# Performance work log

Hardware: AMD Instinct MI355X
Metric: run time of the kernel (lower is better)

Reference implementation:

```python
import jax, jax.numpy as jnp
import numpy as np

N = 100000      # nodes
E = 1600000     # edges
H = 128         # hidden_dim
L = 4           # num_layers (blocks AND inner GGC steps)
G = 512         # graphs in batch
IN = 128        # input_dim
OUT = 16        # output_dim
HS = H // 2     # mlp hidden


def setup_inputs() -> dict:
    key = jax.random.key(0)
    ks = jax.random.split(key, 24)
    s = 0.05
    inp = {
        "node_embed": jax.random.normal(ks[0], (N, IN), dtype=jnp.float32),
        "edge_index": jax.random.randint(ks[1], (2, E), 0, N, dtype=jnp.int32),
        "batch": jnp.sort(jax.random.randint(ks[2], (N,), 0, G, dtype=jnp.int32)),
        # nodeEmbed Linear
        "node_w": jax.random.normal(ks[3], (H, IN), dtype=jnp.float32) * s,
        "node_b": jnp.zeros((H,), dtype=jnp.float32),
        # per-block GatedGraphConv weights: [blocks, steps, H, H]
        "ggc_weight": jax.random.normal(ks[4], (L, L, H, H), dtype=jnp.float32) * s,
        # per-block GRUCell weights (torch layout: [3H, H], gates r,z,n)
        "gru_w_ih": jax.random.normal(ks[5], (L, 3 * H, H), dtype=jnp.float32) * s,
        "gru_w_hh": jax.random.normal(ks[6], (L, 3 * H, H), dtype=jnp.float32) * s,
        "gru_b_ih": jnp.zeros((L, 3 * H), dtype=jnp.float32),
        "gru_b_hh": jnp.zeros((L, 3 * H), dtype=jnp.float32),
        # cat_linear: H*L -> H
        "cat_w": jax.random.normal(ks[7], (H, H * L), dtype=jnp.float32) * s,
        "cat_b": jnp.zeros((H,), dtype=jnp.float32),
        # gate_nn: H -> 1
        "gate_w": jax.random.normal(ks[8], (1, H), dtype=jnp.float32) * s,
        "gate_b": jnp.zeros((1,), dtype=jnp.float32),
        # mlp
        "mlp_w1": jax.random.normal(ks[9], (HS, H), dtype=jnp.float32) * s,
        "mlp_b1": jnp.zeros((HS,), dtype=jnp.float32),
        "mlp_w2": jax.random.normal(ks[10], (HS, HS), dtype=jnp.float32) * s,
        "mlp_b2": jnp.zeros((HS,), dtype=jnp.float32),
        # heads
        "out_w": jax.random.normal(ks[11], (OUT, HS), dtype=jnp.float32) * s,
        "out_b": jnp.zeros((OUT,), dtype=jnp.float32),
        "line_w": jax.random.normal(ks[12], (OUT, H), dtype=jnp.float32) * s,
        "line_b": jnp.zeros((OUT,), dtype=jnp.float32),
    }
    return inp


def _gru_cell(m, h, w_ih, w_hh, b_ih, b_hh):
    gi = m @ w_ih.T + b_ih            # [N, 3H]
    gh = h @ w_hh.T + b_hh            # [N, 3H]
    i_r, i_z, i_n = jnp.split(gi, 3, axis=-1)
    h_r, h_z, h_n = jnp.split(gh, 3, axis=-1)
    r = jax.nn.sigmoid(i_r + h_r)
    z = jax.nn.sigmoid(i_z + h_z)
    n = jnp.tanh(i_n + r * h_n)
    return (1.0 - z) * n + z * h


def _gated_graph_conv(x, src, dst, W, w_ih, w_hh, b_ih, b_hh):
    n = x.shape[0]
    for i in range(W.shape[0]):       # fixed small step count
        m = x @ W[i]                  # [N, H]
        agg = jax.ops.segment_sum(m[src], dst, num_segments=n)  # scatter-add messages
        x = _gru_cell(agg, x, w_ih, w_hh, b_ih, b_hh)
    return x


def reference(node_embed, edge_index, batch, node_w, node_b, ggc_weight,
              gru_w_ih, gru_w_hh, gru_b_ih, gru_b_hh, cat_w, cat_b,
              gate_w, gate_b, mlp_w1, mlp_b1, mlp_w2, mlp_b2,
              out_w, out_b, line_w, line_b):
    src, dst = edge_index[0], edge_index[1]
    h0 = node_embed @ node_w.T + node_b                     # nodeEmbed
    # all residual blocks consume the SAME h0 (per original forward loop)
    outs = [
        _gated_graph_conv(h0, src, dst, ggc_weight[k], gru_w_ih[k],
                          gru_w_hh[k], gru_b_ih[k], gru_b_hh[k]) + h0
        for k in range(ggc_weight.shape[0])
    ]
    hidden = jnp.concatenate(outs, axis=-1) @ cat_w.T + cat_b  # [N, H]
    lineout = hidden @ line_w.T + line_b                       # [N, OUT]
    # attentional aggregation: scatter softmax over per-graph gates
    gate = (hidden @ gate_w.T + gate_b)[:, 0]                  # [N]
    gmax = jax.ops.segment_max(gate, batch, num_segments=G)
    ex = jnp.exp(gate - gmax[batch])
    denom = jax.ops.segment_sum(ex, batch, num_segments=G)
    alpha = ex / denom[batch]
    pooled = jax.ops.segment_sum(alpha[:, None] * hidden, batch, num_segments=G)  # [G, H]
    h = jax.nn.relu(pooled @ mlp_w1.T + mlp_b1)
    h = jax.nn.relu(h @ mlp_w2.T + mlp_b2)
    out = h @ out_w.T + out_b                                  # [G, OUT]
    return (out, lineout)
```

## Files before the change

kernel.cpp:

```cpp
#include <hip/hip_runtime.h>

#define N_NODES 100000
#define N_EDGES 1600000
#define HD 128
#define NH (N_NODES * HD)

typedef __attribute__((ext_vector_type(8))) short bf16x8;
typedef __attribute__((ext_vector_type(4))) float f32x4;

__device__ inline unsigned short f2bf(float f) {
  unsigned u = __float_as_uint(f);
  unsigned r = (u + 0x7FFFu + ((u >> 16) & 1u)) >> 16;
  return (unsigned short)r;
}
__device__ inline float bf2f(unsigned short b) {
  return __uint_as_float(((unsigned)b) << 16);
}
__device__ inline float sigm_f(float x) {
  return __builtin_amdgcn_rcpf(1.f + __expf(-x));
}
__device__ inline float tanh_f(float x) {
  return 1.f - 2.f * __builtin_amdgcn_rcpf(__expf(2.f * x) + 1.f);
}

__global__ __launch_bounds__(256) void gemm_h0_k(
    const float* __restrict__ A, const float* __restrict__ B,
    const float* __restrict__ bias, unsigned short* __restrict__ Cb, int M) {
  __shared__ float As[16][132];
  __shared__ float Bs[16][68];
  const int tid = threadIdx.x;
  const int row0 = blockIdx.x * 128;
  const int col0 = blockIdx.y * 64;
  const int tx = tid & 15, ty = tid >> 4;

  float acc[8][4];
#pragma unroll
  for (int i = 0; i < 8; i++)
#pragma unroll
    for (int j = 0; j < 4; j++) acc[i][j] = 0.f;

  const int lr = tid >> 2;
  const int kg = (tid & 3) * 4;

  for (int k0 = 0; k0 < 128; k0 += 16) {
#pragma unroll
    for (int h = 0; h < 2; ++h) {
      int r = lr + h * 64;
      float4 v = make_float4(0.f, 0.f, 0.f, 0.f);
      if (row0 + r < M)
        v = *reinterpret_cast<const float4*>(A + (size_t)(row0 + r) * 128 + k0 + kg);
      As[kg + 0][r] = v.x;
      As[kg + 1][r] = v.y;
      As[kg + 2][r] = v.z;
      As[kg + 3][r] = v.w;
    }
    {
      int c = lr;
      float4 v = *reinterpret_cast<const float4*>(B + (size_t)(col0 + c) * 128 + k0 + kg);
      Bs[kg + 0][c] = v.x;
      Bs[kg + 1][c] = v.y;
      Bs[kg + 2][c] = v.z;
      Bs[kg + 3][c] = v.w;
    }
    __syncthreads();
#pragma unroll
    for (int kk = 0; kk < 16; ++kk) {
      float a[8], b[4];
#pragma unroll
      for (int i = 0; i < 8; i++) a[i] = As[kk][ty * 8 + i];
#pragma unroll
      for (int j = 0; j < 4; j++) b[j] = Bs[kk][tx * 4 + j];
#pragma unroll
      for (int i = 0; i < 8; i++)
#pragma unroll
        for (int j = 0; j < 4; j++) acc[i][j] += a[i] * b[j];
    }
    __syncthreads();
  }

#pragma unroll
  for (int i = 0; i < 8; i++) {
    int r = row0 + ty * 8 + i;
    if (r < M) {
#pragma unroll
      for (int j = 0; j < 4; j++) {
        int c = col0 + tx * 4 + j;
        Cb[(size_t)r * 128 + c] = f2bf(acc[i][j] + bias[c]);
      }
    }
  }
}

__global__ __launch_bounds__(256) void gemm_wct_k(
    const float* __restrict__ w_ih, const float* __restrict__ ggc_w,
    float* __restrict__ Cout) {
  const int z = blockIdx.z;
  const float* A = w_ih + (size_t)(z >> 2) * 384 * 128;
  const float* B = ggc_w + (size_t)z * 128 * 128;
  float* C = Cout + (size_t)z * 384 * 128;
  __shared__ float As[16][132];
  __shared__ float Bs[16][68];
  const int tid = threadIdx.x;
  const int row0 = blockIdx.x * 128;
  const int col0 = blockIdx.y * 64;
  const int tx = tid & 15, ty = tid >> 4;

  float acc[8][4];
#pragma unroll
  for (int i = 0; i < 8; i++)
#pragma unroll
    for (int j = 0; j < 4; j++) acc[i][j] = 0.f;

  const int lr = tid >> 2;
  const int kg = (tid & 3) * 4;

  for (int k0 = 0; k0 < 128; k0 += 16) {
#pragma unroll
    for (int h = 0; h < 2; ++h) {
      int r = lr + h * 64;
      float4 v = *reinterpret_cast<const float4*>(A + (size_t)(row0 + r) * 128 + k0 + kg);
      As[kg + 0][r] = v.x;
      As[kg + 1][r] = v.y;
      As[kg + 2][r] = v.z;
      As[kg + 3][r] = v.w;
    }
    {
      int c = lr;
      float4 v = *reinterpret_cast<const float4*>(B + (size_t)(col0 + c) * 128 + k0 + kg);
      Bs[kg + 0][c] = v.x;
      Bs[kg + 1][c] = v.y;
      Bs[kg + 2][c] = v.z;
      Bs[kg + 3][c] = v.w;
    }
    __syncthreads();
#pragma unroll
    for (int kk = 0; kk < 16; ++kk) {
      float a[8], b[4];
#pragma unroll
      for (int i = 0; i < 8; i++) a[i] = As[kk][ty * 8 + i];
#pragma unroll
      for (int j = 0; j < 4; j++) b[j] = Bs[kk][tx * 4 + j];
#pragma unroll
      for (int i = 0; i < 8; i++)
#pragma unroll
        for (int j = 0; j < 4; j++) acc[i][j] += a[i] * b[j];
    }
    __syncthreads();
  }

#pragma unroll
  for (int i = 0; i < 8; i++) {
    int r = row0 + ty * 8 + i;
#pragma unroll
    for (int j = 0; j < 4; j++) {
      int c = col0 + tx * 4 + j;
      C[(size_t)r * 128 + c] = acc[i][j];
    }
  }
}

__global__ __launch_bounds__(256) void f2b_k(const float* __restrict__ a,
                                             unsigned short* __restrict__ b, int n) {
  int i = blockIdx.x * 256 + threadIdx.x;
  if (i * 4 >= n) return;
  float4 v = reinterpret_cast<const float4*>(a)[i];
  ushort4 o;
  o.x = f2bf(v.x);
  o.y = f2bf(v.y);
  o.z = f2bf(v.z);
  o.w = f2bf(v.w);
  reinterpret_cast<ushort4*>(b)[i] = o;
}

template <bool LAST>
__global__ __launch_bounds__(256) void gru_mfma5_k(
    const unsigned short* __restrict__ agg_base, size_t agg_zs,
    const unsigned short* __restrict__ xb_base, size_t xstride,
    const unsigned short* __restrict__ h0b,
    const unsigned short* __restrict__ wct_base, size_t wct_zs,
    const unsigned short* __restrict__ whh_base, size_t whh_zs,
    const float* __restrict__ bih_base, const float* __restrict__ bhh_base,
    unsigned short* __restrict__ xbout, int nRowTiles) {
  const int z = blockIdx.z;
  const unsigned short* agg = agg_base + (size_t)z * agg_zs;
  const unsigned short* xb = xb_base + (size_t)z * xstride;
  unsigned short* out = xbout + (size_t)z * NH;
  const unsigned short* wctb = wct_base + (size_t)z * wct_zs;
  const unsigned short* whhb = whh_base + (size_t)z * whh_zs;
  const float* b_ih = bih_base + z * 384;
  const float* b_hh = bhh_base + z * 384;

  const int lane = threadIdx.x & 63;
  const int wave = threadIdx.x >> 6;
  const int lrow = lane & 15;
  const int kblk = lane >> 4;
  const int c = blockIdx.y * 16 + lrow;

  bf16x8 wf[6][4];
#pragma unroll
  for (int s = 0; s < 3; s++)
#pragma unroll
    for (int kk = 0; kk < 4; kk++) {
      size_t off = (size_t)(s * 128 + c) * 128 + kk * 32 + kblk * 8;
      wf[s][kk] = *reinterpret_cast<const bf16x8*>(wctb + off);
      wf[s + 3][kk] = *reinterpret_cast<const bf16x8*>(whhb + off);
    }
  const float bi0 = b_ih[c], bi1 = b_ih[128 + c], bi2 = b_ih[256 + c];
  const float bh0 = b_hh[c], bh1 = b_hh[128 + c], bh2 = b_hh[256 + c];

  const int tstride = gridDim.x * 4;
  for (int rt = blockIdx.x * 4 + wave; rt < nRowTiles; rt += tstride) {
    const int row0 = rt * 16;
    const size_t abase = (size_t)(row0 + lrow) * 128 + kblk * 8;
    const int ob = row0 + kblk * 4;

    unsigned short hxv[4], h0v[4];
#pragma unroll
    for (int r = 0; r < 4; r++) {
      hxv[r] = xb[(size_t)(ob + r) * 128 + c];
      if (LAST) h0v[r] = h0b[(size_t)(ob + r) * 128 + c];
    }

    f32x4 acc[6];
#pragma unroll
    for (int s = 0; s < 6; s++) acc[s] = (f32x4)(0.f);
#pragma unroll
    for (int kk = 0; kk < 4; kk++) {
      bf16x8 a_ag = *reinterpret_cast<const bf16x8*>(agg + abase + kk * 32);
      bf16x8 a_x = *reinterpret_cast<const bf16x8*>(xb + abase + kk * 32);
      acc[0] = __builtin_amdgcn_mfma_f32_16x16x32_bf16(a_ag, wf[0][kk], acc[0], 0, 0, 0);
      acc[1] = __builtin_amdgcn_mfma_f32_16x16x32_bf16(a_ag, wf[1][kk], acc[1], 0, 0, 0);
      acc[2] = __builtin_amdgcn_mfma_f32_16x16x32_bf16(a_ag, wf[2][kk], acc[2], 0, 0, 0);
      acc[3] = __builtin_amdgcn_mfma_f32_16x16x32_bf16(a_x, wf[3][kk], acc[3], 0, 0, 0);
      acc[4] = __builtin_amdgcn_mfma_f32_16x16x32_bf16(a_x, wf[4][kk], acc[4], 0, 0, 0);
      acc[5] = __builtin_amdgcn_mfma_f32_16x16x32_bf16(a_x, wf[5][kk], acc[5], 0, 0, 0);
    }
#pragma unroll
    for (int r = 0; r < 4; r++) {
      size_t idx = (size_t)(ob + r) * 128 + c;
      float ir = acc[0][r] + bi0;
      float iz = acc[1][r] + bi1;
      float in_ = acc[2][r] + bi2;
      float hr = acc[3][r] + bh0;
      float hz = acc[4][r] + bh1;
      float hn = acc[5][r] + bh2;
      float rg = sigm_f(ir + hr);
      float zg = sigm_f(iz + hz);
      float ng = tanh_f(in_ + rg * hn);
      float h = bf2f(hxv[r]);
      float nv = (1.f - zg) * ng + zg * h;
      if (LAST) nv += bf2f(h0v[r]);
      out[idx] = f2bf(nv);
    }
  }
}

__global__ __launch_bounds__(256) void cat_mfma2_k(
    const unsigned short* __restrict__ outs, const unsigned short* __restrict__ wcatb,
    const float* __restrict__ cat_b, float* __restrict__ hidden, int M, int pair) {
  const int lane = threadIdx.x & 63;
  const int wave = threadIdx.x >> 6;
  const int row0 = blockIdx.x * 64 + wave * 16;
  const int c0 = blockIdx.y * 32;
  const int lrow = lane & 15;
  const int kb = lane >> 4;
  int arow = row0 + lrow;
  if (arow >= M) arow = M - 1;

  f32x4 acc[2];
  acc[0] = (f32x4)(0.f);
  acc[1] = (f32x4)(0.f);
#pragma unroll
  for (int kk = 0; kk < 8; kk++) {
    const unsigned short* ob = outs + (size_t)(kk >> 2) * NH;
    bf16x8 a = *reinterpret_cast<const bf16x8*>(
        ob + (size_t)arow * 128 + (kk & 3) * 32 + kb * 8);
#pragma unroll
    for (int t = 0; t < 2; t++) {
      bf16x8 b = *reinterpret_cast<const bf16x8*>(
          wcatb + (size_t)(c0 + t * 16 + lrow) * 512 + pair * 256 + (kk >> 2) * 128 +
          (kk & 3) * 32 + kb * 8);
      acc[t] = __builtin_amdgcn_mfma_f32_16x16x32_bf16(a, b, acc[t], 0, 0, 0);
    }
  }
#pragma unroll
  for (int r = 0; r < 4; r++) {
    int orow = row0 + kb * 4 + r;
    if (orow >= M) continue;
#pragma unroll
    for (int t = 0; t < 2; t++) {
      int c = c0 + t * 16 + lrow;
      size_t idx = (size_t)orow * 128 + c;
      float v = acc[t][r];
      v += (pair == 0) ? cat_b[c] : hidden[idx];
      hidden[idx] = v;
    }
  }
}

__global__ __launch_bounds__(256) void deg_hist_k(const int* __restrict__ dst,
                                                  int* __restrict__ deg) {
  int e = blockIdx.x * 256 + threadIdx.x;
  if (e >= N_EDGES) return;
  atomicAdd(&deg[dst[e]], 1);
}

__global__ __launch_bounds__(256) void scan1_k(const int* __restrict__ deg,
                                               int* __restrict__ offsets,
                                               int* __restrict__ bsum) {
  __shared__ int buf[256];
  int tid = threadIdx.x;
  int idx = blockIdx.x * 256 + tid;
  int v = (idx < N_NODES) ? deg[idx] : 0;
  buf[tid] = v;
  __syncthreads();
  for (int off = 1; off < 256; off <<= 1) {
    int t = (tid >= off) ? buf[tid - off] : 0;
    __syncthreads();
    buf[tid] += t;
    __syncthreads();
  }
  if (idx < N_NODES) offsets[idx] = buf[tid] - v;
  if (tid == 255) bsum[blockIdx.x] = buf[255];
}

__global__ __launch_bounds__(512) void scan2_k(int* __restrict__ bsum, int nb) {
  __shared__ int buf[512];
  int tid = threadIdx.x;
  int v = (tid < nb) ? bsum[tid] : 0;
  buf[tid] = v;
  __syncthreads();
  for (int off = 1; off < 512; off <<= 1) {
    int t = (tid >= off) ? buf[tid - off] : 0;
    __syncthreads();
    buf[tid] += t;
    __syncthreads();
  }
  if (tid < nb) bsum[tid] = buf[tid] - v;
}

__global__ __launch_bounds__(256) void scan3_k(int* __restrict__ offsets,
                                               const int* __restrict__ bsum) {
  int idx = blockIdx.x * 256 + threadIdx.x;
  if (idx < N_NODES) offsets[idx] += bsum[idx >> 8];
  if (idx == 0) offsets[N_NODES] = N_EDGES;
}

__global__ __launch_bounds__(256) void copy_int_k(const int* __restrict__ a,
                                                  int* __restrict__ b, int n) {
  int i = blockIdx.x * 256 + threadIdx.x;
  if (i < n) b[i] = a[i];
}

__global__ __launch_bounds__(256) void fill_k(const int* __restrict__ src,
                                              const int* __restrict__ dst,
                                              int* __restrict__ cursor,
                                              int* __restrict__ srcs_sorted) {
  int e = blockIdx.x * 256 + threadIdx.x;
  if (e >= N_EDGES) return;
  int pos = atomicAdd(&cursor[dst[e]], 1);
  srcs_sorted[pos] = src[e];
}

__global__ __launch_bounds__(256) void gather5_k(
    const unsigned short* __restrict__ xb_base, size_t xstride,
    const int* __restrict__ offsets, const int* __restrict__ srcs,
    unsigned short* __restrict__ aggb, int nz) {
  int wid = (blockIdx.x * 256 + threadIdx.x) >> 6;
  int lane = threadIdx.x & 63;
  if (wid >= nz * N_NODES) return;
  int z = (wid >= N_NODES) ? 1 : 0;
  int node = wid - z * N_NODES;
  const unsigned short* xb = xb_base + (size_t)z * xstride;
  int beg = offsets[node], end = offsets[node + 1];
  int half = lane >> 5;
  int cg = (lane & 31) * 4;
  float a0 = 0.f, a1 = 0.f, a2 = 0.f, a3 = 0.f;
  int e = beg + half;
  for (; e + 6 < end; e += 8) {
    int s0 = srcs[e], s1 = srcs[e + 2], s2 = srcs[e + 4], s3 = srcs[e + 6];
    uint2 v0 = *reinterpret_cast<const uint2*>(xb + (size_t)s0 * 128 + cg);
    uint2 v1 = *reinterpret_cast<const uint2*>(xb + (size_t)s1 * 128 + cg);
    uint2 v2 = *reinterpret_cast<const uint2*>(xb + (size_t)s2 * 128 + cg);
    uint2 v3 = *reinterpret_cast<const uint2*>(xb + (size_t)s3 * 128 + cg);
    a0 += bf2f((unsigned short)(v0.x & 0xFFFFu)) + bf2f((unsigned short)(v1.x & 0xFFFFu)) +
          bf2f((unsigned short)(v2.x & 0xFFFFu)) + bf2f((unsigned short)(v3.x & 0xFFFFu));
    a1 += bf2f((unsigned short)(v0.x >> 16)) + bf2f((unsigned short)(v1.x >> 16)) +
          bf2f((unsigned short)(v2.x >> 16)) + bf2f((unsigned short)(v3.x >> 16));
    a2 += bf2f((unsigned short)(v0.y & 0xFFFFu)) + bf2f((unsigned short)(v1.y & 0xFFFFu)) +
          bf2f((unsigned short)(v2.y & 0xFFFFu)) + bf2f((unsigned short)(v3.y & 0xFFFFu));
    a3 += bf2f((unsigned short)(v0.y >> 16)) + bf2f((unsigned short)(v1.y >> 16)) +
          bf2f((unsigned short)(v2.y >> 16)) + bf2f((unsigned short)(v3.y >> 16));
  }
  for (; e < end; e += 2) {
    int s0 = srcs[e];
    uint2 v0 = *reinterpret_cast<const uint2*>(xb + (size_t)s0 * 128 + cg);
    a0 += bf2f((unsigned short)(v0.x & 0xFFFFu));
    a1 += bf2f((unsigned short)(v0.x >> 16));
    a2 += bf2f((unsigned short)(v0.y & 0xFFFFu));
    a3 += bf2f((unsigned short)(v0.y >> 16));
  }
  a0 += __shfl_down(a0, 32);
  a1 += __shfl_down(a1, 32);
  a2 += __shfl_down(a2, 32);
  a3 += __shfl_down(a3, 32);
  if (half == 0) {
    uint2 o;
    o.x = (unsigned)f2bf(a0) | ((unsigned)f2bf(a1) << 16);
    o.y = (unsigned)f2bf(a2) | ((unsigned)f2bf(a3) << 16);
    *reinterpret_cast<uint2*>(aggb + (size_t)z * NH + (size_t)node * 128 + cg) = o;
  }
}

__global__ __launch_bounds__(256) void lineout_k(
    const float* __restrict__ hidden, const float* __restrict__ W,
    const float* __restrict__ b, float* __restrict__ out) {
  __shared__ float Ws[16 * 128];
  for (int i = threadIdx.x; i < 2048; i += 256) Ws[i] = W[i];
  __syncthreads();
  int r = threadIdx.x >> 4, c = threadIdx.x & 15;
  int n = blockIdx.x * 16 + r;
  if (n >= N_NODES) return;
  const float* h = hidden + (size_t)n * 128;
  const float* w = Ws + c * 128;
  float acc = 0.f;
#pragma unroll 8
  for (int k = 0; k < 128; k++) acc += h[k] * w[k];
  out[(size_t)n * 16 + c] = acc + b[c];
}

__global__ __launch_bounds__(256) void gate_k(
    const float* __restrict__ hidden, const float* __restrict__ gw,
    const float* __restrict__ gb, float* __restrict__ gate) {
  int wid = (blockIdx.x * 256 + threadIdx.x) >> 6;
  int lane = threadIdx.x & 63;
  if (wid >= N_NODES) return;
  const float* h = hidden + (size_t)wid * 128;
  float s = h[lane] * gw[lane] + h[64 + lane] * gw[64 + lane];
#pragma unroll
  for (int off = 32; off; off >>= 1) s += __shfl_down(s, off);
  if (lane == 0) gate[wid] = s + gb[0];
}

__global__ void graph_start_k(const int* __restrict__ batch, int* __restrict__ gs) {
  int g = threadIdx.x;
  if (g > 512) return;
  if (g == 512) {
    gs[512] = N_NODES;
    return;
  }
  int lo = 0, hi = N_NODES;
  while (lo < hi) {
    int mid = (lo + hi) >> 1;
    if (batch[mid] < g) lo = mid + 1;
    else hi = mid;
  }
  gs[g] = lo;
}

__global__ __launch_bounds__(256) void pool_fused_k(
    const float* __restrict__ hidden, const float* __restrict__ gate,
    const int* __restrict__ gs, float* __restrict__ ex,
    float* __restrict__ pooled) {
  const int g = blockIdx.x;
  const int beg = gs[g], end = gs[g + 1];
  const int tid = threadIdx.x, lane = tid & 63, wv = tid >> 6;
  __shared__ float red[4];
  __shared__ float sval;
  __shared__ float colbuf[256];

  if (end <= beg) {
    if (tid < 128) pooled[(size_t)g * 128 + tid] = 0.f;
    return;
  }
  float m = -3.4e38f;
  for (int n = beg + tid; n < end; n += 256) m = fmaxf(m, gate[n]);
#pragma unroll
  for (int off = 32; off; off >>= 1) m = fmaxf(m, __shfl_down(m, off));
  if (lane == 0) red[wv] = m;
  __syncthreads();
  if (tid == 0) sval = fmaxf(fmaxf(red[0], red[1]), fmaxf(red[2], red[3]));
  __syncthreads();
  const float mx = sval;
  float s = 0.f;
  for (int n = beg + tid; n < end; n += 256) {
    float e = __expf(gate[n] - mx);
    ex[n] = e;
    s += e;
  }
#pragma unroll
  for (int off = 32; off; off >>= 1) s += __shfl_down(s, off);
  if (lane == 0) red[wv] = s;
  __syncthreads();
  if (tid == 0) sval = red[0] + red[1] + red[2] + red[3];
  __syncthreads();
  const float denom = sval;
  const int col = tid & 127, half = tid >> 7;
  float acc = 0.f;
  for (int n = beg + half; n < end; n += 2)
    acc += ex[n] * hidden[(size_t)n * 128 + col];
  colbuf[tid] = acc;
  __syncthreads();
  if (tid < 128)
    pooled[(size_t)g * 128 + tid] = (colbuf[tid] + colbuf[tid + 128]) / denom;
}

__global__ void mlp1_k(const float* __restrict__ pooled, const float* __restrict__ w,
                       const float* __restrict__ b, float* __restrict__ h1) {
  int g = blockIdx.x, j = threadIdx.x;
  const float* p = pooled + (size_t)g * 128;
  const float* wr = w + (size_t)j * 128;
  float acc = 0.f;
#pragma unroll 8
  for (int k = 0; k < 128; k++) acc += p[k] * wr[k];
  acc += b[j];
  h1[g * 64 + j] = acc > 0.f ? acc : 0.f;
}

__global__ void mlp2_k(const float* __restrict__ h1, const float* __restrict__ w,
                       const float* __restrict__ b, float* __restrict__ h2) {
  int g = blockIdx.x, j = threadIdx.x;
  const float* p = h1 + (size_t)g * 64;
  const float* wr = w + (size_t)j * 64;
  float acc = 0.f;
#pragma unroll 8
  for (int k = 0; k < 64; k++) acc += p[k] * wr[k];
  acc += b[j];
  h2[g * 64 + j] = acc > 0.f ? acc : 0.f;
}

__global__ void outhead_k(const float* __restrict__ h2, const float* __restrict__ w,
                          const float* __restrict__ b, float* __restrict__ out) {
  int g = blockIdx.x, j = threadIdx.x;
  if (j >= 16) return;
  const float* p = h2 + (size_t)g * 64;
  const float* wr = w + (size_t)j * 64;
  float acc = 0.f;
#pragma unroll 8
  for (int k = 0; k < 64; k++) acc += p[k] * wr[k];
  out[g * 16 + j] = acc + b[j];
}

extern "C" void kernel_launch(void* const* d_in, const int* in_sizes, int n_in,
                              void* d_out, int out_size, void* d_ws, size_t ws_size,
                              hipStream_t stream) {
  const float* node_embed = (const float*)d_in[0];
  const int* eidx = (const int*)d_in[1];
  const int* batch = (const int*)d_in[2];
  const float* node_w = (const float*)d_in[3];
  const float* node_b = (const float*)d_in[4];
  const float* ggc_w = (const float*)d_in[5];
  const float* w_ih = (const float*)d_in[6];
  const float* w_hh = (const float*)d_in[7];
  const float* b_ih = (const float*)d_in[8];
  const float* b_hh = (const float*)d_in[9];
  const float* cat_w = (const float*)d_in[10];
  const float* cat_b = (const float*)d_in[11];
  const float* gate_w = (const float*)d_in[12];
  const float* gate_b = (const float*)d_in[13];
  const float* mlp_w1 = (const float*)d_in[14];
  const float* mlp_b1 = (const float*)d_in[15];
  const float* mlp_w2 = (const float*)d_in[16];
  const float* mlp_b2 = (const float*)d_in[17];
  const float* out_w = (const float*)d_in[18];
  const float* out_b = (const float*)d_in[19];
  const float* line_w = (const float*)d_in[20];
  const float* line_b = (const float*)d_in[21];

  const int* src = eidx;
  const int* dst = eidx + N_EDGES;

  float* hidden = (float*)d_ws;
  unsigned short* h0b = (unsigned short*)(hidden + (size_t)NH);
  unsigned short* X0 = h0b + (size_t)NH;
  unsigned short* X1 = X0 + (size_t)2 * NH;
  unsigned short* aggb = X1 + (size_t)2 * NH;
  unsigned short* wctb = aggb + (size_t)2 * NH;
  unsigned short* whhb = wctb + 16 * 384 * 128;
  unsigned short* wcatb = whhb + 4 * 384 * 128;
  int* offsets = (int*)(wcatb + 128 * 512);
  int* cursor = offsets + N_NODES + 1;
  int* srcs_sorted = cursor + N_NODES;
  int* bsum = srcs_sorted + N_EDGES;
  int* gs = bsum + 512;
  float* WcTf = (float*)aggb;

  float* out_graph = (float*)d_out;
  float* out_line = (float*)d_out + 512 * 16;

  dim3 blk(256);
  const int gM128 = (N_NODES + 127) / 128;
  const int gM64 = (N_NODES + 63) / 64;
  const int gE = (N_EDGES + 255) / 256;
  const int nScanBlk = (N_NODES + 255) / 256;
  const int nRowTiles = N_NODES / 16;
  const size_t S = (size_t)384 * 128;

  hipMemsetAsync(cursor, 0, N_NODES * sizeof(int), stream);
  deg_hist_k<<<gE, blk, 0, stream>>>(dst, cursor);
  scan1_k<<<nScanBlk, blk, 0, stream>>>(cursor, offsets, bsum);
  scan2_k<<<1, 512, 0, stream>>>(bsum, nScanBlk);
  scan3_k<<<nScanBlk, blk, 0, stream>>>(offsets, bsum);
  copy_int_k<<<(N_NODES + 255) / 256, blk, 0, stream>>>(offsets, cursor, N_NODES);
  fill_k<<<gE, blk, 0, stream>>>(src, dst, cursor, srcs_sorted);
  graph_start_k<<<1, 576, 0, stream>>>(batch, gs);

  gemm_wct_k<<<dim3(3, 2, 16), blk, 0, stream>>>(w_ih, ggc_w, WcTf);
  f2b_k<<<(16 * 384 * 128 / 4 + 255) / 256, blk, 0, stream>>>(WcTf, wctb, 16 * 384 * 128);
  f2b_k<<<(4 * 384 * 128 / 4 + 255) / 256, blk, 0, stream>>>(w_hh, whhb, 4 * 384 * 128);
  f2b_k<<<(128 * 512 / 4 + 255) / 256, blk, 0, stream>>>(cat_w, wcatb, 128 * 512);

  gemm_h0_k<<<dim3(gM128, 2), blk, 0, stream>>>(node_embed, node_w, node_b, h0b, N_NODES);

  const int gGather2 = (2 * N_NODES * 64 + 255) / 256;
  const int gGather1 = (N_NODES * 64 + 255) / 256;
  const dim3 gruGrid(400, 8, 2);
  for (int p = 0; p < 2; p++) {
    const float* bih_p = b_ih + (size_t)p * 2 * 384;
    const float* bhh_p = b_hh + (size_t)p * 2 * 384;
    const unsigned short* whh_p = whhb + (size_t)p * 2 * S;
    for (int i = 0; i < 4; i++) {
      const unsigned short* wct_pi = wctb + ((size_t)8 * p + i) * S;
      const unsigned short* xin;
      size_t xs;
      unsigned short* xout;
      if (i == 0) { xin = h0b; xs = 0; xout = X0; }
      else if (i == 1) { xin = X0; xs = NH; xout = X1; }
      else if (i == 2) { xin = X1; xs = NH; xout = X0; }
      else { xin = X0; xs = NH; xout = X1; }
      const size_t agg_zs = (i == 0) ? 0 : (size_t)NH;
      gather5_k<<<(i == 0 ? gGather1 : gGather2), blk, 0, stream>>>(
          xin, xs, offsets, srcs_sorted, aggb, (i == 0 ? 1 : 2));
      if (i < 3)
        gru_mfma5_k<false><<<gruGrid, blk, 0, stream>>>(
            aggb, agg_zs, xin, xs, h0b, wct_pi, 4 * S, whh_p, S, bih_p, bhh_p,
            xout, nRowTiles);
      else
        gru_mfma5_k<true><<<gruGrid, blk, 0, stream>>>(
            aggb, agg_zs, xin, xs, h0b, wct_pi, 4 * S, whh_p, S, bih_p, bhh_p,
            xout, nRowTiles);
    }
    cat_mfma2_k<<<dim3(gM64, 4), blk, 0, stream>>>(X1, wcatb, cat_b, hidden, N_NODES, p);
  }

  lineout_k<<<(N_NODES + 15) / 16, blk, 0, stream>>>(hidden, line_w, line_b, out_line);

  float* gate = (float*)X0;
  float* ex = (float*)X0 + N_NODES;
  float* pooled = (float*)aggb;
  float* h1 = pooled + 512 * 128;
  float* h2 = h1 + 512 * 64;

  gate_k<<<(N_NODES * 64 + 255) / 256, blk, 0, stream>>>(hidden, gate_w, gate_b, gate);
  pool_fused_k<<<512, blk, 0, stream>>>(hidden, gate, gs, ex, pooled);
  mlp1_k<<<512, 64, 0, stream>>>(pooled, mlp_w1, mlp_b1, h1);
  mlp2_k<<<512, 64, 0, stream>>>(h1, mlp_w2, mlp_b2, h2);
  outhead_k<<<512, 64, 0, stream>>>(h2, out_w, out_b, out_graph);
}
```

Before: 2.796 ms.

## Batch all four GGC blocks per step with in-place GRU and single cat GEMM

Runs the four residual GatedGraphConv blocks together, as z=4 in one gather launch and one GRU launch per step, instead of two passes of two blocks each. Each GRU block now has 8 waves covering all 128 output columns of one 16-row tile, and it updates the X buffer in place; a __syncthreads keeps every wave's operand loads ahead of the writes. The concat linear becomes a single K=512 MFMA GEMM, with no partial accumulation into hidden. The aim is fewer kernel launches, more parallel work per launch and less read-modify-write traffic on hidden, at the cost of a smaller GRU grid (512 blocks) and a larger workspace footprint.

```diff
diff --git a/kernel.cpp b/kernel.cpp
--- a/kernel.cpp
+++ b/kernel.cpp
@@ -173,18 +173,18 @@
 }
 
 template <bool LAST>
-__global__ __launch_bounds__(256) void gru_mfma5_k(
+__global__ __launch_bounds__(512) void gru_mfma7_k(
     const unsigned short* __restrict__ agg_base, size_t agg_zs,
-    const unsigned short* __restrict__ xb_base, size_t xstride,
+    const unsigned short* __restrict__ xb_base, size_t xb_zs,
     const unsigned short* __restrict__ h0b,
     const unsigned short* __restrict__ wct_base, size_t wct_zs,
     const unsigned short* __restrict__ whh_base, size_t whh_zs,
     const float* __restrict__ bih_base, const float* __restrict__ bhh_base,
-    unsigned short* __restrict__ xbout, int nRowTiles) {
-  const int z = blockIdx.z;
+    unsigned short* __restrict__ Xout, int nRowTiles) {
+  const int z = blockIdx.y;
   const unsigned short* agg = agg_base + (size_t)z * agg_zs;
-  const unsigned short* xb = xb_base + (size_t)z * xstride;
-  unsigned short* out = xbout + (size_t)z * NH;
+  const unsigned short* xb = xb_base + (size_t)z * xb_zs;
+  unsigned short* out = Xout + (size_t)z * NH;
   const unsigned short* wctb = wct_base + (size_t)z * wct_zs;
   const unsigned short* whhb = whh_base + (size_t)z * whh_zs;
   const float* b_ih = bih_base + z * 384;
@@ -194,7 +194,7 @@
   const int wave = threadIdx.x >> 6;
   const int lrow = lane & 15;
   const int kblk = lane >> 4;
-  const int c = blockIdx.y * 16 + lrow;
+  const int c = wave * 16 + lrow;
 
   bf16x8 wf[6][4];
 #pragma unroll
@@ -208,18 +208,9 @@
   const float bi0 = b_ih[c], bi1 = b_ih[128 + c], bi2 = b_ih[256 + c];
   const float bh0 = b_hh[c], bh1 = b_hh[128 + c], bh2 = b_hh[256 + c];
 
-  const int tstride = gridDim.x * 4;
-  for (int rt = blockIdx.x * 4 + wave; rt < nRowTiles; rt += tstride) {
+  for (int rt = blockIdx.x; rt < nRowTiles; rt += gridDim.x) {
     const int row0 = rt * 16;
     const size_t abase = (size_t)(row0 + lrow) * 128 + kblk * 8;
-    const int ob = row0 + kblk * 4;
-
-    unsigned short hxv[4], h0v[4];
-#pragma unroll
-    for (int r = 0; r < 4; r++) {
-      hxv[r] = xb[(size_t)(ob + r) * 128 + c];
-      if (LAST) h0v[r] = h0b[(size_t)(ob + r) * 128 + c];
-    }
 
     f32x4 acc[6];
 #pragma unroll
@@ -235,9 +226,11 @@
       acc[4] = __builtin_amdgcn_mfma_f32_16x16x32_bf16(a_x, wf[4][kk], acc[4], 0, 0, 0);
       acc[5] = __builtin_amdgcn_mfma_f32_16x16x32_bf16(a_x, wf[5][kk], acc[5], 0, 0, 0);
     }
+    __syncthreads();
 #pragma unroll
     for (int r = 0; r < 4; r++) {
-      size_t idx = (size_t)(ob + r) * 128 + c;
+      int orow = row0 + kblk * 4 + r;
+      size_t idx = (size_t)orow * 128 + c;
       float ir = acc[0][r] + bi0;
       float iz = acc[1][r] + bi1;
       float in_ = acc[2][r] + bi2;
@@ -247,17 +240,18 @@
       float rg = sigm_f(ir + hr);
       float zg = sigm_f(iz + hz);
       float ng = tanh_f(in_ + rg * hn);
-      float h = bf2f(hxv[r]);
+      float h = bf2f(xb[idx]);
       float nv = (1.f - zg) * ng + zg * h;
-      if (LAST) nv += bf2f(h0v[r]);
+      if (LAST) nv += bf2f(h0b[idx]);
       out[idx] = f2bf(nv);
     }
   }
 }
 
-__global__ __launch_bounds__(256) void cat_mfma2_k(
-    const unsigned short* __restrict__ outs, const unsigned short* __restrict__ wcatb,
-    const float* __restrict__ cat_b, float* __restrict__ hidden, int M, int pair) {
+__global__ __launch_bounds__(256) void cat_full_k(
+    const unsigned short* __restrict__ X,
+    const unsigned short* __restrict__ wcatb,
+    const float* __restrict__ cat_b, float* __restrict__ hidden, int M) {
   const int lane = threadIdx.x & 63;
   const int wave = threadIdx.x >> 6;
   const int row0 = blockIdx.x * 64 + wave * 16;
@@ -271,14 +265,14 @@
   acc[0] = (f32x4)(0.f);
   acc[1] = (f32x4)(0.f);
 #pragma unroll
-  for (int kk = 0; kk < 8; kk++) {
-    const unsigned short* ob = outs + (size_t)(kk >> 2) * NH;
+  for (int kk = 0; kk < 16; kk++) {
+    const unsigned short* ob = X + (size_t)(kk >> 2) * NH;
     bf16x8 a = *reinterpret_cast<const bf16x8*>(
         ob + (size_t)arow * 128 + (kk & 3) * 32 + kb * 8);
 #pragma unroll
     for (int t = 0; t < 2; t++) {
       bf16x8 b = *reinterpret_cast<const bf16x8*>(
-          wcatb + (size_t)(c0 + t * 16 + lrow) * 512 + pair * 256 + (kk >> 2) * 128 +
+          wcatb + (size_t)(c0 + t * 16 + lrow) * 512 + (kk >> 2) * 128 +
           (kk & 3) * 32 + kb * 8);
       acc[t] = __builtin_amdgcn_mfma_f32_16x16x32_bf16(a, b, acc[t], 0, 0, 0);
     }
@@ -290,10 +284,7 @@
 #pragma unroll
     for (int t = 0; t < 2; t++) {
       int c = c0 + t * 16 + lrow;
-      size_t idx = (size_t)orow * 128 + c;
-      float v = acc[t][r];
-      v += (pair == 0) ? cat_b[c] : hidden[idx];
-      hidden[idx] = v;
+      hidden[(size_t)orow * 128 + c] = acc[t][r] + cat_b[c];
     }
   }
 }
@@ -369,8 +360,9 @@
   int wid = (blockIdx.x * 256 + threadIdx.x) >> 6;
   int lane = threadIdx.x & 63;
   if (wid >= nz * N_NODES) return;
-  int z = (wid >= N_NODES) ? 1 : 0;
-  int node = wid - z * N_NODES;
+  int z = 0, node = wid;
+  if (node >= 2 * N_NODES) { z = 2; node -= 2 * N_NODES; }
+  if (node >= N_NODES) { z += 1; node -= N_NODES; }
   const unsigned short* xb = xb_base + (size_t)z * xstride;
   int beg = offsets[node], end = offsets[node + 1];
   int half = lane >> 5;
@@ -570,12 +562,10 @@
   const int* src = eidx;
   const int* dst = eidx + N_EDGES;
 
-  float* hidden = (float*)d_ws;
-  unsigned short* h0b = (unsigned short*)(hidden + (size_t)NH);
-  unsigned short* X0 = h0b + (size_t)NH;
-  unsigned short* X1 = X0 + (size_t)2 * NH;
-  unsigned short* aggb = X1 + (size_t)2 * NH;
-  unsigned short* wctb = aggb + (size_t)2 * NH;
+  unsigned short* h0b = (unsigned short*)d_ws;
+  unsigned short* X = h0b + (size_t)NH;
+  unsigned short* aggb = X + (size_t)4 * NH;
+  unsigned short* wctb = aggb + (size_t)4 * NH;
   unsigned short* whhb = wctb + 16 * 384 * 128;
   unsigned short* wcatb = whhb + 4 * 384 * 128;
   int* offsets = (int*)(wcatb + 128 * 512);
@@ -584,6 +574,7 @@
   int* bsum = srcs_sorted + N_EDGES;
   int* gs = bsum + 512;
   float* WcTf = (float*)aggb;
+  float* hidden = (float*)aggb;
 
   float* out_graph = (float*)d_out;
   float* out_line = (float*)d_out + 512 * 16;
@@ -612,42 +603,32 @@
 
   gemm_h0_k<<<dim3(gM128, 2), blk, 0, stream>>>(node_embed, node_w, node_b, h0b, N_NODES);
 
-  const int gGather2 = (2 * N_NODES * 64 + 255) / 256;
-  const int gGather1 = (N_NODES * 64 + 255) / 256;
-  const dim3 gruGrid(400, 8, 2);
-  for (int p = 0; p < 2; p++) {
-    const float* bih_p = b_ih + (size_t)p * 2 * 384;
-    const float* bhh_p = b_hh + (size_t)p * 2 * 384;
-    const unsigned short* whh_p = whhb + (size_t)p * 2 * S;
-    for (int i = 0; i < 4; i++) {
-      const unsigned short* wct_pi = wctb + ((size_t)8 * p + i) * S;
-      const unsigned short* xin;
-      size_t xs;
-      unsigned short* xout;
-      if (i == 0) { xin = h0b; xs = 0; xout = X0; }
-      else if (i == 1) { xin = X0; xs = NH; xout = X1; }
-      else if (i == 2) { xin = X1; xs = NH; xout = X0; }
-      else { xin = X0; xs = NH; xout = X1; }
-      const size_t agg_zs = (i == 0) ? 0 : (size_t)NH;
-      gather5_k<<<(i == 0 ? gGather1 : gGather2), blk, 0, stream>>>(
-          xin, xs, offsets, srcs_sorted, aggb, (i == 0 ? 1 : 2));
-      if (i < 3)
-        gru_mfma5_k<false><<<gruGrid, blk, 0, stream>>>(
-            aggb, agg_zs, xin, xs, h0b, wct_pi, 4 * S, whh_p, S, bih_p, bhh_p,
-            xout, nRowTiles);
-      else
-        gru_mfma5_k<true><<<gruGrid, blk, 0, stream>>>(
-            aggb, agg_zs, xin, xs, h0b, wct_pi, 4 * S, whh_p, S, bih_p, bhh_p,
-            xout, nRowTiles);
-    }
-    cat_mfma2_k<<<dim3(gM64, 4), blk, 0, stream>>>(X1, wcatb, cat_b, hidden, N_NODES, p);
-  }
+  const dim3 gruGrid(128, 4);
+  for (int i = 0; i < 4; i++) {
+    const unsigned short* xin = (i == 0) ? h0b : X;
+    const size_t xzs = (i == 0) ? 0 : (size_t)NH;
+    const int nz = (i == 0) ? 1 : 4;
+    const size_t agg_zs = (i == 0) ? 0 : (size_t)NH;
+    gather5_k<<<(nz * N_NODES * 64 + 255) / 256, blk, 0, stream>>>(
+        xin, xzs, offsets, srcs_sorted, aggb, nz);
+    const unsigned short* wct_i = wctb + (size_t)i * S;
+    if (i < 3)
+      gru_mfma7_k<false><<<gruGrid, 512, 0, stream>>>(
+          aggb, agg_zs, xin, xzs, h0b, wct_i, 4 * S, whhb, S, b_ih, b_hh, X,
+          nRowTiles);
+    else
+      gru_mfma7_k<true><<<gruGrid, 512, 0, stream>>>(
+          aggb, agg_zs, xin, xzs, h0b, wct_i, 4 * S, whhb, S, b_ih, b_hh, X,
+          nRowTiles);
+  }
+
+  cat_full_k<<<dim3(gM64, 4), blk, 0, stream>>>(X, wcatb, cat_b, hidden, N_NODES);
 
   lineout_k<<<(N_NODES + 15) / 16, blk, 0, stream>>>(hidden, line_w, line_b, out_line);
 
-  float* gate = (float*)X0;
-  float* ex = (float*)X0 + N_NODES;
-  float* pooled = (float*)aggb;
+  float* gate = (float*)X;
+  float* ex = (float*)X + N_NODES;
+  float* pooled = hidden + (size_t)NH;
   float* h1 = pooled + 512 * 128;
   float* h2 = h1 + 512 * 64;
 
```

Measured after the change: 2.296 ms. 1.22x faster.
